# Optimization experiments

Measured on AMD Instinct MI355X. Metric: run time of the kernel, lower is better.

The kernel has to match this reference:

```python
import jax, jax.numpy as jnp
import numpy as np

N = 100000
E = 1600000
EPS = 1e-5


def setup_inputs() -> dict:
    key = jax.random.key(0)
    ks = jax.random.split(key, 6)
    x = jax.random.normal(ks[0], (N, 128), dtype=jnp.float32)
    edge_index = jax.random.randint(ks[1], (2, E), 0, N, dtype=jnp.int64)
    # Glorot-ish scaled weights
    W1 = jax.random.normal(ks[2], (128, 128), dtype=jnp.float32) * (1.0 / np.sqrt(128))
    b1 = jnp.zeros((128,), dtype=jnp.float32)
    gamma = jnp.ones((128,), dtype=jnp.float32)
    beta = jnp.zeros((128,), dtype=jnp.float32)
    W2 = jax.random.normal(ks[3], (64, 128), dtype=jnp.float32) * (1.0 / np.sqrt(128))
    b2 = jnp.zeros((64,), dtype=jnp.float32)
    return {"x": x, "edge_index": edge_index, "W1": W1, "b1": b1,
            "gamma": gamma, "beta": beta, "W2": W2, "b2": b2}


def _gcn_conv(x, W, b, src, dst, norm, n):
    # x: [N, Fin], W: [Fout, Fin] -> h: [N, Fout]
    h = x @ W.T
    msg = h[src] * norm[:, None]               # [E+N, Fout] gather + scale
    out = jax.ops.segment_sum(msg, dst, num_segments=n)  # scatter-add
    return out + b


def reference(x, edge_index, W1, b1, gamma, beta, W2, b2):
    n = x.shape[0]
    loop = jnp.arange(n, dtype=edge_index.dtype)
    src = jnp.concatenate([edge_index[0], loop])   # self-loops appended
    dst = jnp.concatenate([edge_index[1], loop])
    # symmetric normalization D^-1/2 A D^-1/2 (degree at destination)
    deg = jax.ops.segment_sum(jnp.ones_like(dst, dtype=x.dtype), dst, num_segments=n)
    dis = jnp.where(deg > 0, jax.lax.rsqrt(deg), 0.0)
    norm = dis[src] * dis[dst]

    h = _gcn_conv(x, W1, b1, src, dst, norm, n)
    # BatchNorm1d (training mode: biased batch statistics over nodes)
    mean = jnp.mean(h, axis=0)
    var = jnp.mean((h - mean) ** 2, axis=0)
    h = (h - mean) * jax.lax.rsqrt(var + EPS) * gamma + beta
    h = jax.nn.relu(h)
    out = _gcn_conv(h, W2, b2, src, dst, norm, n)
    return out
```

## Files before the change

### kernel.cpp

```cpp
#include <hip/hip_runtime.h>


#define SHIFT 8
#define BSZ   256
#define CHUNK 4096
#define EPT   (CHUNK/256)
#define NBMAX 1024

typedef short bf16x8 __attribute__((ext_vector_type(8)));
typedef float f32x4  __attribute__((ext_vector_type(4)));

__device__ __forceinline__ unsigned short f2bf(float f) {
    unsigned int u = __float_as_uint(f);
    unsigned int r = (u + 0x7FFFu + ((u >> 16) & 1u)) >> 16;
    return (unsigned short)r;
}
__device__ __forceinline__ float bf2f(unsigned short h) {
    return __uint_as_float(((unsigned int)h) << 16);
}
__device__ __forceinline__ void split2(float a, float b, unsigned int& hi, unsigned int& lo) {
    unsigned int ua = __float_as_uint(a), ub = __float_as_uint(b);
    unsigned int ha = ua & 0xFFFF0000u,  hb = ub & 0xFFFF0000u;
    hi = (ha >> 16) | hb;
    float la = a - __uint_as_float(ha);
    float lb = b - __uint_as_float(hb);
    lo = (__float_as_uint(la) >> 16) | (__float_as_uint(lb) & 0xFFFF0000u);
}
__device__ __forceinline__ int detect64(const int* __restrict__ p) {
    int o = 0;
#pragma unroll
    for (int q = 0; q < 16; ++q) o |= p[2 * q + 1];
    return (o == 0) ? 1 : 0;
}

__global__ __launch_bounds__(256) void k_hist(const void* __restrict__ eiv,
                                              int* __restrict__ gcnt,
                                              int E, int N, int NB) {
    __shared__ int h[NBMAX];
    int t = threadIdx.x;
    for (int u = t; u < NB; u += 256) h[u] = 0;
    __syncthreads();
    int base = blockIdx.x * CHUNK;
    int f = detect64((const int*)eiv);
    const long long* e64 = (const long long*)eiv;
    const int*       e32 = (const int*)eiv;
#pragma unroll
    for (int r = 0; r < EPT; ++r) {
        int e = base + r * 256 + t;
        if (e < E) {
            int s, d;
            if (f) { s = (int)e64[e]; d = (int)e64[E + e]; }
            else   { s = e32[e];      d = e32[E + e]; }
            if ((unsigned)s < (unsigned)N && (unsigned)d < (unsigned)N)
                atomicAdd(&h[d >> SHIFT], 1);
        }
    }
    __syncthreads();
    for (int u = t; u < NB; u += 256) {
        int c = h[u];
        if (c) atomicAdd(&gcnt[u], c);
    }
}

__global__ void k_scan(const int* __restrict__ gcnt, int* __restrict__ gbase,
                       int* __restrict__ gcur, int NB) {
    __shared__ int sh[1024];
    int t = threadIdx.x;
    int v = (t < NB) ? gcnt[t] : 0;
    sh[t] = v;
    __syncthreads();
    for (int off = 1; off < 1024; off <<= 1) {
        int x = sh[t];
        int y = (t >= off) ? sh[t - off] : 0;
        __syncthreads();
        sh[t] = x + y;
        __syncthreads();
    }
    if (t < NB) {
        int ex = sh[t] - v;
        gbase[t] = ex;
        gcur[t]  = ex;
    }
    if (t == 0) gbase[NB] = sh[1023];
}

__global__ __launch_bounds__(256) void k_scatter(const void* __restrict__ eiv,
                                                 int* __restrict__ gcur,
                                                 unsigned int* __restrict__ ebuf,
                                                 int E, int N, int NB) {
    __shared__ int lcnt[NBMAX];
    __shared__ int lbase[NBMAX];
    int t = threadIdx.x;
    for (int u = t; u < NB; u += 256) lcnt[u] = 0;
    __syncthreads();
    int base = blockIdx.x * CHUNK;
    int f = detect64((const int*)eiv);
    const long long* e64 = (const long long*)eiv;
    const int*       e32 = (const int*)eiv;
    unsigned int ent[EPT];
    int bk[EPT];
    int off[EPT];
#pragma unroll
    for (int r = 0; r < EPT; ++r) {
        int e = base + r * 256 + t;
        bk[r] = -1;
        if (e < E) {
            int s, d;
            if (f) { s = (int)e64[e]; d = (int)e64[E + e]; }
            else   { s = e32[e];      d = e32[E + e]; }
            if ((unsigned)s < (unsigned)N && (unsigned)d < (unsigned)N) {
                int b = d >> SHIFT;
                bk[r]  = b;
                off[r] = atomicAdd(&lcnt[b], 1);
                ent[r] = ((unsigned int)(d & (BSZ - 1)) << 24) | (unsigned int)s;
            }
        }
    }
    __syncthreads();
    for (int u = t; u < NB; u += 256) {
        int c = lcnt[u];
        lbase[u] = c ? atomicAdd(&gcur[u], c) : 0;
    }
    __syncthreads();
#pragma unroll
    for (int r = 0; r < EPT; ++r)
        if (bk[r] >= 0) ebuf[(size_t)lbase[bk[r]] + off[r]] = ent[r];
}

__global__ __launch_bounds__(256) void k_fine(const unsigned int* __restrict__ ebuf,
                                              const int* __restrict__ gbase,
                                              int* __restrict__ cnt,
                                              float* __restrict__ dis,
                                              int* __restrict__ rowptr,
                                              int* __restrict__ elist, int N) {
    __shared__ int lc[BSZ];
    __shared__ int ls[BSZ];
    int t = threadIdx.x;
    int b = blockIdx.x;
    int start = gbase[b], end = gbase[b + 1];
    int m = end - start;
    lc[t] = 0;
    __syncthreads();
    for (int j = t; j < m; j += 256)
        atomicAdd(&lc[ebuf[start + j] >> 24], 1);
    __syncthreads();
    int v = lc[t];
    ls[t] = v;
    __syncthreads();
    for (int off = 1; off < BSZ; off <<= 1) {
        int x = ls[t];
        int y = (t >= off) ? ls[t - off] : 0;
        __syncthreads();
        ls[t] = x + y;
        __syncthreads();
    }
    int ex = ls[t] - v;
    int i = (b << SHIFT) + t;
    if (i < N) {
        cnt[i]    = v;
        dis[i]    = rsqrtf((float)v + 1.0f);
        rowptr[i] = start + ex;
    }
    lc[t] = ex;
    __syncthreads();
    for (int j = t; j < m; j += 256) {
        unsigned int e = ebuf[start + j];
        int p = atomicAdd(&lc[e >> 24], 1);
        elist[start + p] = (int)(e & 0xFFFFFFu);
    }
}

__global__ __launch_bounds__(256) void k_prepw(const float* __restrict__ W1,
                                               const float* __restrict__ W2,
                                               uint4* __restrict__ Whi1,
                                               uint4* __restrict__ Wlo1,
                                               uint4* __restrict__ Whi2,
                                               uint4* __restrict__ Wlo2) {
    int idx = blockIdx.x * 256 + threadIdx.x;
    const float* W; uint4 *H, *L; int slot;
    if (idx < 2048)      { W = W1; H = Whi1; L = Wlo1; slot = idx; }
    else if (idx < 3072) { W = W2; H = Whi2; L = Wlo2; slot = idx - 2048; }
    else return;
    int lane = slot & 63, kt = (slot >> 6) & 3, nt = slot >> 8;
    int o = nt * 16 + (lane & 15);
    int k0 = kt * 32 + (lane >> 4) * 8;
    const float* p = W + (size_t)o * 128 + k0;
    unsigned int h[4], l[4];
#pragma unroll
    for (int pr = 0; pr < 4; ++pr) split2(p[2 * pr], p[2 * pr + 1], h[pr], l[pr]);
    H[slot] = make_uint4(h[0], h[1], h[2], h[3]);
    L[slot] = make_uint4(l[0], l[1], l[2], l[3]);
}

__global__ __launch_bounds__(256) void k_gemm1(const float* __restrict__ x,
                                               const uint4* __restrict__ Whi,
                                               const uint4* __restrict__ Wlo,
                                               const float* __restrict__ dis,
                                               unsigned short* __restrict__ h1b, int N) {
    __shared__ uint4 Ahi[1024];
    __shared__ uint4 Alo[1024];
    int t = threadIdx.x;
    int n0 = blockIdx.x * 64;
    for (int s = t; s < 1024; s += 256) {
        int lane = s & 63, kt = (s >> 6) & 3, c = s >> 8;
        int row = n0 + c * 16 + (lane & 15);
        int rr = min(row, N - 1);
        int k0 = kt * 32 + (lane >> 4) * 8;
        const float4* p = (const float4*)(x + (size_t)rr * 128 + k0);
        float4 u0 = p[0], u1 = p[1];
        unsigned int h0, h1, h2, h3, l0, l1, l2, l3;
        split2(u0.x, u0.y, h0, l0);
        split2(u0.z, u0.w, h1, l1);
        split2(u1.x, u1.y, h2, l2);
        split2(u1.z, u1.w, h3, l3);
        Ahi[s] = make_uint4(h0, h1, h2, h3);
        Alo[s] = make_uint4(l0, l1, l2, l3);
    }
    __syncthreads();
    int w = t >> 6, lane = t & 63;
    bf16x8 ah[4], al[4];
#pragma unroll
    for (int kt = 0; kt < 4; ++kt) {
        ah[kt] = ((const bf16x8*)Ahi)[(w * 4 + kt) * 64 + lane];
        al[kt] = ((const bf16x8*)Alo)[(w * 4 + kt) * 64 + lane];
    }
    f32x4 acc[8];
#pragma unroll
    for (int nt = 0; nt < 8; ++nt) {
        acc[nt] = (f32x4)(0.f);
#pragma unroll
        for (int kt = 0; kt < 4; ++kt) {
            bf16x8 bh = ((const bf16x8*)Whi)[(nt * 4 + kt) * 64 + lane];
            bf16x8 bl = ((const bf16x8*)Wlo)[(nt * 4 + kt) * 64 + lane];
            acc[nt] = __builtin_amdgcn_mfma_f32_16x16x32_bf16(ah[kt], bh, acc[nt], 0, 0, 0);
            acc[nt] = __builtin_amdgcn_mfma_f32_16x16x32_bf16(ah[kt], bl, acc[nt], 0, 0, 0);
            acc[nt] = __builtin_amdgcn_mfma_f32_16x16x32_bf16(al[kt], bh, acc[nt], 0, 0, 0);
        }
    }
    int r0 = n0 + w * 16 + (lane >> 4) * 4;
    float dv[4];
#pragma unroll
    for (int r = 0; r < 4; ++r) {
        int row = r0 + r;
        dv[r] = (row < N) ? dis[row] : 0.f;
    }
#pragma unroll
    for (int nt = 0; nt < 8; ++nt) {
        int col = nt * 16 + (lane & 15);
#pragma unroll
        for (int r = 0; r < 4; ++r) {
            int row = r0 + r;
            if (row < N) h1b[(size_t)row * 128 + col] = f2bf(dv[r] * acc[nt][r]);
        }
    }
}

__global__ __launch_bounds__(256) void k_agg1(const unsigned int* __restrict__ h1b,
                                              const float* __restrict__ dis,
                                              const int* __restrict__ rowptr,
                                              const int* __restrict__ cnt,
                                              const int* __restrict__ elist,
                                              float* __restrict__ agg1,
                                              float* __restrict__ spart, int N) {
    int t = threadIdx.x;
    int lane = t & 63;
    int i0 = blockIdx.x * 16 + (t >> 6) * 4;
    float sx = 0.f, sy = 0.f, qx = 0.f, qy = 0.f;
#pragma unroll
    for (int k = 0; k < 4; ++k) {
        int i = i0 + k;
        bool act = (i < N);
        float accx = 0.f, accy = 0.f;
        int base = 0, c = 0;
        if (act) { base = rowptr[i]; c = cnt[i]; }
        int j = 0;
        for (; j + 16 <= c; j += 16) {
            int ss[16];
#pragma unroll
            for (int r = 0; r < 16; ++r) ss[r] = elist[base + j + r];
            unsigned int vv[16];
#pragma unroll
            for (int r = 0; r < 16; ++r) vv[r] = h1b[(size_t)ss[r] * 64 + lane];
#pragma unroll
            for (int r = 0; r < 16; ++r) {
                accx += bf2f((unsigned short)(vv[r] & 0xFFFF));
                accy += bf2f((unsigned short)(vv[r] >> 16));
            }
        }
        if (j + 8 <= c) {
            int ss[8];
#pragma unroll
            for (int r = 0; r < 8; ++r) ss[r] = elist[base + j + r];
            unsigned int vv[8];
#pragma unroll
            for (int r = 0; r < 8; ++r) vv[r] = h1b[(size_t)ss[r] * 64 + lane];
#pragma unroll
            for (int r = 0; r < 8; ++r) {
                accx += bf2f((unsigned short)(vv[r] & 0xFFFF));
                accy += bf2f((unsigned short)(vv[r] >> 16));
            }
            j += 8;
        }
        for (; j < c; ++j) {
            int s = elist[base + j];
            unsigned int v = h1b[(size_t)s * 64 + lane];
            accx += bf2f((unsigned short)(v & 0xFFFF));
            accy += bf2f((unsigned short)(v >> 16));
        }
        if (act) {
            float di = dis[i];
            unsigned int sv = h1b[(size_t)i * 64 + lane];
            float rx = di * (accx + bf2f((unsigned short)(sv & 0xFFFF)));
            float ry = di * (accy + bf2f((unsigned short)(sv >> 16)));
            ((float2*)agg1)[(size_t)i * 64 + lane] = make_float2(rx, ry);
            sx += rx; sy += ry; qx += rx * rx; qy += ry * ry;
        }
    }
    __shared__ float4 red[256];
    red[t] = make_float4(sx, sy, qx, qy);
    __syncthreads();
    if (t < 64) {
        float4 a = red[t], b = red[t + 64], cc = red[t + 128], d = red[t + 192];
        float ssx = a.x + b.x + cc.x + d.x;
        float ssy = a.y + b.y + cc.y + d.y;
        float sqx = a.z + b.z + cc.z + d.z;
        float sqy = a.w + b.w + cc.w + d.w;
        float* sp = spart + ((size_t)(blockIdx.x & 63) << 8);
        atomicAdd(&sp[2 * t],           ssx);
        atomicAdd(&sp[2 * t + 1],       ssy);
        atomicAdd(&sp[128 + 2 * t],     sqx);
        atomicAdd(&sp[128 + 2 * t + 1], sqy);
    }
}

__global__ void k_bnfin(const float* __restrict__ spart, float* __restrict__ stats,
                        const float* __restrict__ gamma,
                        const float* __restrict__ beta, int N) {
    __shared__ float sred[256];
    int t = threadIdx.x;
    float s = 0.f;
    for (int sl = 0; sl < 64; ++sl) s += spart[sl * 256 + t];
    sred[t] = s;
    __syncthreads();
    if (t < 128) {
        float invN = 1.0f / (float)N;
        float mean = sred[t] * invN;
        float var = sred[128 + t] * invN - mean * mean;
        var = fmaxf(var, 0.f);
        float inv = rsqrtf(var + 1e-5f);
        float sc = gamma[t] * inv;
        stats[256 + t] = sc;
        stats[384 + t] = beta[t] - mean * sc;
    }
}

__global__ __launch_bounds__(256) void k_gemm2(const float* __restrict__ agg1,
                                               const uint4* __restrict__ Whi,
                                               const uint4* __restrict__ Wlo,
                                               const float* __restrict__ stats,
                                               const float* __restrict__ dis,
                                               unsigned short* __restrict__ h2b, int N) {
    __shared__ uint4 Ahi[1024];
    __shared__ uint4 Alo[1024];
    int t = threadIdx.x;
    int n0 = blockIdx.x * 64;
    const float4* st = (const float4*)stats;
    for (int s = t; s < 1024; s += 256) {
        int lane = s & 63, kt = (s >> 6) & 3, c = s >> 8;
        int row = n0 + c * 16 + (lane & 15);
        int rr = min(row, N - 1);
        int k0 = kt * 32 + (lane >> 4) * 8;
        const float4* p = (const float4*)(agg1 + (size_t)rr * 128 + k0);
        float4 a0 = p[0], a1 = p[1];
        float4 c0 = st[64 + (k0 >> 2)], c1 = st[65 + (k0 >> 2)];
        float4 s0 = st[96 + (k0 >> 2)], s1 = st[97 + (k0 >> 2)];
        float v0 = fmaxf(a0.x * c0.x + s0.x, 0.f);
        float v1 = fmaxf(a0.y * c0.y + s0.y, 0.f);
        float v2 = fmaxf(a0.z * c0.z + s0.z, 0.f);
        float v3 = fmaxf(a0.w * c0.w + s0.w, 0.f);
        float v4 = fmaxf(a1.x * c1.x + s1.x, 0.f);
        float v5 = fmaxf(a1.y * c1.y + s1.y, 0.f);
        float v6 = fmaxf(a1.z * c1.z + s1.z, 0.f);
        float v7 = fmaxf(a1.w * c1.w + s1.w, 0.f);
        unsigned int h0, h1, h2, h3, l0, l1, l2, l3;
        split2(v0, v1, h0, l0);
        split2(v2, v3, h1, l1);
        split2(v4, v5, h2, l2);
        split2(v6, v7, h3, l3);
        Ahi[s] = make_uint4(h0, h1, h2, h3);
        Alo[s] = make_uint4(l0, l1, l2, l3);
    }
    __syncthreads();
    int w = t >> 6, lane = t & 63;
    bf16x8 ah[4], al[4];
#pragma unroll
    for (int kt = 0; kt < 4; ++kt) {
        ah[kt] = ((const bf16x8*)Ahi)[(w * 4 + kt) * 64 + lane];
        al[kt] = ((const bf16x8*)Alo)[(w * 4 + kt) * 64 + lane];
    }
    f32x4 acc[4];
#pragma unroll
    for (int nt = 0; nt < 4; ++nt) {
        acc[nt] = (f32x4)(0.f);
#pragma unroll
        for (int kt = 0; kt < 4; ++kt) {
            bf16x8 bh = ((const bf16x8*)Whi)[(nt * 4 + kt) * 64 + lane];
            bf16x8 bl = ((const bf16x8*)Wlo)[(nt * 4 + kt) * 64 + lane];
            acc[nt] = __builtin_amdgcn_mfma_f32_16x16x32_bf16(ah[kt], bh, acc[nt], 0, 0, 0);
            acc[nt] = __builtin_amdgcn_mfma_f32_16x16x32_bf16(ah[kt], bl, acc[nt], 0, 0, 0);
            acc[nt] = __builtin_amdgcn_mfma_f32_16x16x32_bf16(al[kt], bh, acc[nt], 0, 0, 0);
        }
    }
    int r0 = n0 + w * 16 + (lane >> 4) * 4;
    float dv[4];
#pragma unroll
    for (int r = 0; r < 4; ++r) {
        int row = r0 + r;
        dv[r] = (row < N) ? dis[row] : 0.f;
    }
#pragma unroll
    for (int nt = 0; nt < 4; ++nt) {
        int col = nt * 16 + (lane & 15);
#pragma unroll
        for (int r = 0; r < 4; ++r) {
            int row = r0 + r;
            if (row < N) h2b[(size_t)row * 64 + col] = f2bf(dv[r] * acc[nt][r]);
        }
    }
}

__global__ __launch_bounds__(256) void k_agg2(const unsigned short* __restrict__ h2b,
                                              const float* __restrict__ dis,
                                              const int* __restrict__ rowptr,
                                              const int* __restrict__ cnt,
                                              const int* __restrict__ elist,
                                              const float* __restrict__ b2,
                                              float* __restrict__ out, int N) {
    int lane = threadIdx.x & 63;
    int i = blockIdx.x * 4 + (threadIdx.x >> 6);
    if (i >= N) return;
    float acc = 0.f;
    int base = rowptr[i], c = cnt[i];
    int j = 0;
    for (; j + 16 <= c; j += 16) {
        int ss[16];
#pragma unroll
        for (int r = 0; r < 16; ++r) ss[r] = elist[base + j + r];
        unsigned short vv[16];
#pragma unroll
        for (int r = 0; r < 16; ++r) vv[r] = h2b[(size_t)ss[r] * 64 + lane];
#pragma unroll
        for (int r = 0; r < 16; ++r) acc += bf2f(vv[r]);
    }
    if (j + 8 <= c) {
        int ss[8];
#pragma unroll
        for (int r = 0; r < 8; ++r) ss[r] = elist[base + j + r];
        unsigned short vv[8];
#pragma unroll
        for (int r = 0; r < 8; ++r) vv[r] = h2b[(size_t)ss[r] * 64 + lane];
#pragma unroll
        for (int r = 0; r < 8; ++r) acc += bf2f(vv[r]);
        j += 8;
    }
    for (; j < c; ++j) {
        int s = elist[base + j];
        acc += bf2f(h2b[(size_t)s * 64 + lane]);
    }
    float di = dis[i];
    float self = bf2f(h2b[(size_t)i * 64 + lane]);
    out[(size_t)i * 64 + lane] = di * (acc + self) + b2[lane];
}

extern "C" void kernel_launch(void* const* d_in, const int* in_sizes, int n_in,
                              void* d_out, int out_size, void* d_ws, size_t ws_size,
                              hipStream_t stream) {
    const float* x     = (const float*)d_in[0];
    const void*  ei    = d_in[1];
    const float* W1    = (const float*)d_in[2];
    const float* gamma = (const float*)d_in[4];
    const float* beta  = (const float*)d_in[5];
    const float* W2    = (const float*)d_in[6];
    const float* b2    = (const float*)d_in[7];
    float* out = (float*)d_out;

    int N = in_sizes[0] / 128;
    int E = in_sizes[1] / 2;
    int NB = (N + BSZ - 1) >> SHIFT;

    size_t Na = ((size_t)N + 3) & ~(size_t)3;
    size_t Ea = ((size_t)E + 3) & ~(size_t)3;
    int*   cnt    = (int*)d_ws;
    int*   rowptr = cnt + Na;
    int*   gcnt   = rowptr + Na;
    int*   gbase  = gcnt + 1024;
    int*   gcur   = gbase + 1028;
    float* stats  = (float*)(gcur + 1024);
    float* spart  = stats + 512;
    float* dis    = spart + 65536;
    int*   elist  = (int*)(dis + Na);
    unsigned int* h1b = (unsigned int*)(elist + Ea);
    float* agg1   = (float*)(h1b + Na * 64);
    unsigned int* ebuf = (unsigned int*)agg1;
    uint4* Whi1   = (uint4*)(agg1 + Na * 128);
    uint4* Wlo1   = Whi1 + 2048;
    uint4* Whi2   = Wlo1 + 2048;
    uint4* Wlo2   = Whi2 + 1024;
    unsigned int* h2b = h1b;

    hipMemsetAsync(gcnt, 0, 1024 * sizeof(int), stream);
    hipMemsetAsync(spart, 0, 16384 * sizeof(float), stream);

    int gC    = (E + CHUNK - 1) / CHUNK;
    int gG1   = (N + 63) / 64;
    int gAgg1 = (N + 15) / 16;
    int gAgg2 = (N + 3) / 4;

    k_prepw<<<12, 256, 0, stream>>>(W1, W2, Whi1, Wlo1, Whi2, Wlo2);
    k_hist<<<gC, 256, 0, stream>>>(ei, gcnt, E, N, NB);
    k_scan<<<1, 1024, 0, stream>>>(gcnt, gbase, gcur, NB);
    k_scatter<<<gC, 256, 0, stream>>>(ei, gcur, ebuf, E, N, NB);
    k_fine<<<NB, 256, 0, stream>>>(ebuf, gbase, cnt, dis, rowptr, elist, N);
    k_gemm1<<<gG1, 256, 0, stream>>>(x, Whi1, Wlo1, dis, (unsigned short*)h1b, N);
    k_agg1<<<gAgg1, 256, 0, stream>>>(h1b, dis, rowptr, cnt, elist, agg1, spart, N);
    k_bnfin<<<1, 256, 0, stream>>>(spart, stats, gamma, beta, N);
    k_gemm2<<<gG1, 256, 0, stream>>>(agg1, Whi2, Wlo2, stats, dis, (unsigned short*)h2b, N);
    k_agg2<<<gAgg2, 256, 0, stream>>>((const unsigned short*)h2b, dis, rowptr, cnt, elist, b2, out, N);
}
```

Before: 384.9 us.

## Fuse graph-build stages into one cooperative kernel with grid syncs

Replaces the weight prep, histogram, scan, scatter and fine-sort kernels plus two memsets with a single cooperative kernel that uses grid-wide syncs between phases. Edge data is read once and kept in registers across the histogram and scatter phases rather than being loaded again. This removes several launches and one pass over the edge list. In exchange it adds grid.sync overhead, requires all blocks to be co-resident (about 391 blocks here), and the scan in block 0 assumes NB is at most 1024.

New measurement: 722.4 us. 1.88x slower.

```diff
diff --git a/kernel.cpp b/kernel.cpp
--- a/kernel.cpp
+++ b/kernel.cpp
@@ -1,4 +1,7 @@
 #include <hip/hip_runtime.h>
+#include <hip/hip_cooperative_groups.h>
+
+namespace cg = cooperative_groups;
 
 
 #define SHIFT 8
@@ -33,67 +36,53 @@
     return (o == 0) ? 1 : 0;
 }
 
-__global__ __launch_bounds__(256) void k_hist(const void* __restrict__ eiv,
-                                              int* __restrict__ gcnt,
-                                              int E, int N, int NB) {
-    __shared__ int h[NBMAX];
-    int t = threadIdx.x;
-    for (int u = t; u < NB; u += 256) h[u] = 0;
-    __syncthreads();
-    int base = blockIdx.x * CHUNK;
-    int f = detect64((const int*)eiv);
-    const long long* e64 = (const long long*)eiv;
-    const int*       e32 = (const int*)eiv;
-#pragma unroll
-    for (int r = 0; r < EPT; ++r) {
-        int e = base + r * 256 + t;
-        if (e < E) {
-            int s, d;
-            if (f) { s = (int)e64[e]; d = (int)e64[E + e]; }
-            else   { s = e32[e];      d = e32[E + e]; }
-            if ((unsigned)s < (unsigned)N && (unsigned)d < (unsigned)N)
-                atomicAdd(&h[d >> SHIFT], 1);
-        }
-    }
-    __syncthreads();
-    for (int u = t; u < NB; u += 256) {
-        int c = h[u];
-        if (c) atomicAdd(&gcnt[u], c);
-    }
-}
-
-__global__ void k_scan(const int* __restrict__ gcnt, int* __restrict__ gbase,
-                       int* __restrict__ gcur, int NB) {
-    __shared__ int sh[1024];
-    int t = threadIdx.x;
-    int v = (t < NB) ? gcnt[t] : 0;
-    sh[t] = v;
-    __syncthreads();
-    for (int off = 1; off < 1024; off <<= 1) {
-        int x = sh[t];
-        int y = (t >= off) ? sh[t - off] : 0;
-        __syncthreads();
-        sh[t] = x + y;
-        __syncthreads();
-    }
-    if (t < NB) {
-        int ex = sh[t] - v;
-        gbase[t] = ex;
-        gcur[t]  = ex;
-    }
-    if (t == 0) gbase[NB] = sh[1023];
-}
-
-__global__ __launch_bounds__(256) void k_scatter(const void* __restrict__ eiv,
-                                                 int* __restrict__ gcur,
-                                                 unsigned int* __restrict__ ebuf,
-                                                 int E, int N, int NB) {
+__global__ __launch_bounds__(256) void k_build(const void* __restrict__ eiv,
+                                               int E, int N, int NB,
+                                               int* __restrict__ gcnt,
+                                               int* __restrict__ gbase,
+                                               int* __restrict__ gcur,
+                                               unsigned int* __restrict__ ebuf,
+                                               int* __restrict__ cnt,
+                                               float* __restrict__ dis,
+                                               int* __restrict__ rowptr,
+                                               int* __restrict__ elist,
+                                               const float* __restrict__ W1,
+                                               const float* __restrict__ W2,
+                                               uint4* __restrict__ Whi1,
+                                               uint4* __restrict__ Wlo1,
+                                               uint4* __restrict__ Whi2,
+                                               uint4* __restrict__ Wlo2,
+                                               float* __restrict__ spart) {
+    cg::grid_group grid = cg::this_grid();
     __shared__ int lcnt[NBMAX];
     __shared__ int lbase[NBMAX];
-    int t = threadIdx.x;
+    __shared__ int ssum[256];
+    int t = threadIdx.x, b = blockIdx.x;
+    int stride = gridDim.x * 256;
+    int gid = b * 256 + t;
+
+    for (int u = gid; u < 1024; u += stride) gcnt[u] = 0;
+    for (int u = gid; u < 16384; u += stride) spart[u] = 0.f;
+    if (b < 12) {
+        int idx = gid;
+        const float* W = 0; uint4 *H = 0, *L = 0; int slot = -1;
+        if (idx < 2048)      { W = W1; H = Whi1; L = Wlo1; slot = idx; }
+        else if (idx < 3072) { W = W2; H = Whi2; L = Wlo2; slot = idx - 2048; }
+        if (slot >= 0) {
+            int lane = slot & 63, kt = (slot >> 6) & 3, nt = slot >> 8;
+            int o = nt * 16 + (lane & 15);
+            int k0 = kt * 32 + (lane >> 4) * 8;
+            const float* p = W + (size_t)o * 128 + k0;
+            unsigned int h[4], l[4];
+#pragma unroll
+            for (int pr = 0; pr < 4; ++pr) split2(p[2 * pr], p[2 * pr + 1], h[pr], l[pr]);
+            H[slot] = make_uint4(h[0], h[1], h[2], h[3]);
+            L[slot] = make_uint4(l[0], l[1], l[2], l[3]);
+        }
+    }
     for (int u = t; u < NB; u += 256) lcnt[u] = 0;
     __syncthreads();
-    int base = blockIdx.x * CHUNK;
+    int base = b * CHUNK;
     int f = detect64((const int*)eiv);
     const long long* e64 = (const long long*)eiv;
     const int*       e32 = (const int*)eiv;
@@ -109,14 +98,46 @@
             if (f) { s = (int)e64[e]; d = (int)e64[E + e]; }
             else   { s = e32[e];      d = e32[E + e]; }
             if ((unsigned)s < (unsigned)N && (unsigned)d < (unsigned)N) {
-                int b = d >> SHIFT;
-                bk[r]  = b;
-                off[r] = atomicAdd(&lcnt[b], 1);
+                int bb = d >> SHIFT;
+                bk[r]  = bb;
+                off[r] = atomicAdd(&lcnt[bb], 1);
                 ent[r] = ((unsigned int)(d & (BSZ - 1)) << 24) | (unsigned int)s;
             }
         }
     }
-    __syncthreads();
+    __threadfence();
+    grid.sync();
+
+    for (int u = t; u < NB; u += 256) {
+        int c = lcnt[u];
+        if (c) atomicAdd(&gcnt[u], c);
+    }
+    __threadfence();
+    grid.sync();
+
+    if (b == 0) {
+        int v0 = gcnt[4 * t], v1 = gcnt[4 * t + 1], v2 = gcnt[4 * t + 2], v3 = gcnt[4 * t + 3];
+        int tsum = v0 + v1 + v2 + v3;
+        ssum[t] = tsum;
+        __syncthreads();
+        for (int o = 1; o < 256; o <<= 1) {
+            int x = ssum[t];
+            int y = (t >= o) ? ssum[t - o] : 0;
+            __syncthreads();
+            ssum[t] = x + y;
+            __syncthreads();
+        }
+        int ex = ssum[t] - tsum;
+        int e0 = ex, e1 = ex + v0, e2 = e1 + v1, e3 = e2 + v2;
+        gbase[4 * t] = e0;  gcur[4 * t] = e0;
+        gbase[4 * t + 1] = e1; gcur[4 * t + 1] = e1;
+        gbase[4 * t + 2] = e2; gcur[4 * t + 2] = e2;
+        gbase[4 * t + 3] = e3; gcur[4 * t + 3] = e3;
+        if (t == 255) gbase[NB] = ssum[255];
+    }
+    __threadfence();
+    grid.sync();
+
     for (int u = t; u < NB; u += 256) {
         int c = lcnt[u];
         lbase[u] = c ? atomicAdd(&gcur[u], c) : 0;
@@ -125,71 +146,42 @@
 #pragma unroll
     for (int r = 0; r < EPT; ++r)
         if (bk[r] >= 0) ebuf[(size_t)lbase[bk[r]] + off[r]] = ent[r];
-}
-
-__global__ __launch_bounds__(256) void k_fine(const unsigned int* __restrict__ ebuf,
-                                              const int* __restrict__ gbase,
-                                              int* __restrict__ cnt,
-                                              float* __restrict__ dis,
-                                              int* __restrict__ rowptr,
-                                              int* __restrict__ elist, int N) {
-    __shared__ int lc[BSZ];
-    __shared__ int ls[BSZ];
-    int t = threadIdx.x;
-    int b = blockIdx.x;
-    int start = gbase[b], end = gbase[b + 1];
-    int m = end - start;
-    lc[t] = 0;
-    __syncthreads();
-    for (int j = t; j < m; j += 256)
-        atomicAdd(&lc[ebuf[start + j] >> 24], 1);
-    __syncthreads();
-    int v = lc[t];
-    ls[t] = v;
-    __syncthreads();
-    for (int off = 1; off < BSZ; off <<= 1) {
-        int x = ls[t];
-        int y = (t >= off) ? ls[t - off] : 0;
+    __threadfence();
+    grid.sync();
+
+    if (b < NB) {
+        int start = gbase[b], end = gbase[b + 1];
+        int m = end - start;
+        lcnt[t] = 0;
         __syncthreads();
-        ls[t] = x + y;
+        for (int j = t; j < m; j += 256)
+            atomicAdd(&lcnt[ebuf[start + j] >> 24], 1);
         __syncthreads();
-    }
-    int ex = ls[t] - v;
-    int i = (b << SHIFT) + t;
-    if (i < N) {
-        cnt[i]    = v;
-        dis[i]    = rsqrtf((float)v + 1.0f);
-        rowptr[i] = start + ex;
-    }
-    lc[t] = ex;
-    __syncthreads();
-    for (int j = t; j < m; j += 256) {
-        unsigned int e = ebuf[start + j];
-        int p = atomicAdd(&lc[e >> 24], 1);
-        elist[start + p] = (int)(e & 0xFFFFFFu);
-    }
-}
-
-__global__ __launch_bounds__(256) void k_prepw(const float* __restrict__ W1,
-                                               const float* __restrict__ W2,
-                                               uint4* __restrict__ Whi1,
-                                               uint4* __restrict__ Wlo1,
-                                               uint4* __restrict__ Whi2,
-                                               uint4* __restrict__ Wlo2) {
-    int idx = blockIdx.x * 256 + threadIdx.x;
-    const float* W; uint4 *H, *L; int slot;
-    if (idx < 2048)      { W = W1; H = Whi1; L = Wlo1; slot = idx; }
-    else if (idx < 3072) { W = W2; H = Whi2; L = Wlo2; slot = idx - 2048; }
-    else return;
-    int lane = slot & 63, kt = (slot >> 6) & 3, nt = slot >> 8;
-    int o = nt * 16 + (lane & 15);
-    int k0 = kt * 32 + (lane >> 4) * 8;
-    const float* p = W + (size_t)o * 128 + k0;
-    unsigned int h[4], l[4];
-#pragma unroll
-    for (int pr = 0; pr < 4; ++pr) split2(p[2 * pr], p[2 * pr + 1], h[pr], l[pr]);
-    H[slot] = make_uint4(h[0], h[1], h[2], h[3]);
-    L[slot] = make_uint4(l[0], l[1], l[2], l[3]);
+        int v = lcnt[t];
+        lbase[t] = v;
+        __syncthreads();
+        for (int o = 1; o < BSZ; o <<= 1) {
+            int x = lbase[t];
+            int y = (t >= o) ? lbase[t - o] : 0;
+            __syncthreads();
+            lbase[t] = x + y;
+            __syncthreads();
+        }
+        int ex = lbase[t] - v;
+        int i = (b << SHIFT) + t;
+        if (i < N) {
+            cnt[i]    = v;
+            dis[i]    = rsqrtf((float)v + 1.0f);
+            rowptr[i] = start + ex;
+        }
+        lcnt[t] = ex;
+        __syncthreads();
+        for (int j = t; j < m; j += 256) {
+            unsigned int e = ebuf[start + j];
+            int p = atomicAdd(&lcnt[e >> 24], 1);
+            elist[start + p] = (int)(e & 0xFFFFFFu);
+        }
+    }
 }
 
 __global__ __launch_bounds__(256) void k_gemm1(const float* __restrict__ x,
@@ -508,19 +500,22 @@
     uint4* Wlo2   = Whi2 + 1024;
     unsigned int* h2b = h1b;
 
-    hipMemsetAsync(gcnt, 0, 1024 * sizeof(int), stream);
-    hipMemsetAsync(spart, 0, 16384 * sizeof(float), stream);
-
     int gC    = (E + CHUNK - 1) / CHUNK;
+    int gB    = gC > NB ? gC : NB;
+    if (gB < 12) gB = 12;
     int gG1   = (N + 63) / 64;
     int gAgg1 = (N + 15) / 16;
     int gAgg2 = (N + 3) / 4;
 
-    k_prepw<<<12, 256, 0, stream>>>(W1, W2, Whi1, Wlo1, Whi2, Wlo2);
-    k_hist<<<gC, 256, 0, stream>>>(ei, gcnt, E, N, NB);
-    k_scan<<<1, 1024, 0, stream>>>(gcnt, gbase, gcur, NB);
-    k_scatter<<<gC, 256, 0, stream>>>(ei, gcur, ebuf, E, N, NB);
-    k_fine<<<NB, 256, 0, stream>>>(ebuf, gbase, cnt, dis, rowptr, elist, N);
+    void* bargs[] = { (void*)&ei, (void*)&E, (void*)&N, (void*)&NB,
+                      (void*)&gcnt, (void*)&gbase, (void*)&gcur, (void*)&ebuf,
+                      (void*)&cnt, (void*)&dis, (void*)&rowptr, (void*)&elist,
+                      (void*)&W1, (void*)&W2,
+                      (void*)&Whi1, (void*)&Wlo1, (void*)&Whi2, (void*)&Wlo2,
+                      (void*)&spart };
+    hipLaunchCooperativeKernel((const void*)k_build, dim3(gB), dim3(256),
+                               bargs, 0, stream);
+
     k_gemm1<<<gG1, 256, 0, stream>>>(x, Whi1, Wlo1, dis, (unsigned short*)h1b, N);
     k_agg1<<<gAgg1, 256, 0, stream>>>(h1b, dis, rowptr, cnt, elist, agg1, spart, N);
     k_bnfin<<<1, 256, 0, stream>>>(spart, stats, gamma, beta, N);
```
